# Kernel optimization log

Hardware: AMD Instinct MI355X
Metric: run time of the kernel (lower is better)

Reference implementation:

```python
import jax, jax.numpy as jnp
import numpy as np

B, S, HID = 2, 2048, 3584
H, KV, D = 16, 8, 256
RQ, RK, RV = 6, 2, 2
GRP = H // KV
EPS = 1e-6
SOFTCAP = 50.0
SCALE = 256.0 ** -0.5  # query_pre_attn_scalar ** -0.5
NEG = -2.3819763e38


def _rmsnorm(x, w):
    # Gemma RMSNorm: fp32 normalize, scale by (1 + weight)
    xf = x.astype(jnp.float32)
    n = xf * jax.lax.rsqrt(jnp.mean(xf * xf, axis=-1, keepdims=True) + EPS)
    return (n * (1.0 + w)).astype(x.dtype)


def _rope_factor(x, freqs_cis):
    # x: [B,S,R,D]; freqs_cis: [S, D/2, 2] = (cos, sin)
    h = D // 2
    cos = freqs_cis[None, :, None, :, 0]  # [1,S,1,D/2]
    sin = freqs_cis[None, :, None, :, 1]
    x1, x2 = x[..., :h], x[..., h:]
    return jnp.concatenate([x1 * cos - x2 * sin, x2 * cos + x1 * sin], axis=-1)


def setup_inputs() -> dict:
    key = jax.random.key(0)
    ks = jax.random.split(key, 10)
    hidden_states = jax.random.normal(ks[0], (B, S, HID), dtype=jnp.float32)
    # rotary tables
    pos = jnp.arange(S, dtype=jnp.float32)
    inv = 1.0 / (10000.0 ** (jnp.arange(0, D, 2, dtype=jnp.float32) / D))
    ang = pos[:, None] * inv[None, :]                     # [S, D/2]
    freqs_cis = jnp.stack([jnp.cos(ang), jnp.sin(ang)], axis=-1)  # [S,D/2,2]
    kv_write_indices = jnp.arange(S, dtype=jnp.int32)
    k_cache_A = jnp.zeros((B, S, KV, RK), jnp.float32)
    k_cache_B = jnp.zeros((B, S, RK, D), jnp.float32)
    v_cache_A = jnp.zeros((B, S, KV, RV), jnp.float32)
    v_cache_B = jnp.zeros((B, S, RV, D), jnp.float32)
    causal = jnp.tril(jnp.ones((S, S), bool))
    mask = jnp.where(causal, 0.0, NEG)[None, None].astype(jnp.float32)
    sd = 1.0 / np.sqrt(HID)
    W_A_q = jax.random.normal(ks[1], (HID, H * RQ), jnp.float32) * sd
    W_A_k = jax.random.normal(ks[2], (HID, KV * RK), jnp.float32) * sd
    W_A_v = jax.random.normal(ks[3], (HID, KV * RV), jnp.float32) * sd
    W_B_q = jax.random.normal(ks[4], (HID, RQ * D), jnp.float32) * sd
    W_B_k = jax.random.normal(ks[5], (HID, RK * D), jnp.float32) * sd
    W_B_v = jax.random.normal(ks[6], (HID, RV * D), jnp.float32) * sd
    o_proj_w = jax.random.normal(ks[7], (H * D, HID), jnp.float32) * (1.0 / np.sqrt(H * D))
    q_norm_w = jnp.zeros((D,), jnp.float32)
    k_norm_w = jnp.zeros((D,), jnp.float32)
    return dict(hidden_states=hidden_states, freqs_cis=freqs_cis,
                kv_write_indices=kv_write_indices,
                k_cache_A=k_cache_A, k_cache_B=k_cache_B,
                v_cache_A=v_cache_A, v_cache_B=v_cache_B, mask=mask,
                W_A_q=W_A_q, W_A_k=W_A_k, W_A_v=W_A_v,
                W_B_q=W_B_q, W_B_k=W_B_k, W_B_v=W_B_v,
                o_proj_w=o_proj_w, q_norm_w=q_norm_w, k_norm_w=k_norm_w)


def reference(hidden_states, freqs_cis, kv_write_indices,
              k_cache_A, k_cache_B, v_cache_A, v_cache_B, mask,
              W_A_q, W_A_k, W_A_v, W_B_q, W_B_k, W_B_v,
              o_proj_w, q_norm_w, k_norm_w):
    hs = hidden_states
    # rank-factor projections (many small GEMMs)
    A_q = (hs @ W_A_q).reshape(B, S, H, RQ)
    A_k = (hs @ W_A_k).reshape(B, S, KV, RK)
    A_v = (hs @ W_A_v).reshape(B, S, KV, RV)
    B_q = (hs @ W_B_q).reshape(B, S, RQ, D)
    B_k = (hs @ W_B_k).reshape(B, S, RK, D)
    B_v = (hs @ W_B_v).reshape(B, S, RV, D)
    # qk-norm on low-rank B factors
    B_q = _rmsnorm(B_q, q_norm_w)
    B_k = _rmsnorm(B_k, k_norm_w)
    # RoPE on factors
    B_q = _rope_factor(B_q, freqs_cis)
    B_k = _rope_factor(B_k, freqs_cis)
    # factored KV cache write (prefill: indices = arange(S))
    kA = k_cache_A.at[:, kv_write_indices].set(A_k)
    kB = k_cache_B.at[:, kv_write_indices].set(B_k)
    vA = v_cache_A.at[:, kv_write_indices].set(A_v)
    vB = v_cache_B.at[:, kv_write_indices].set(B_v)
    # reconstruct Q/K/V from rank-R tensor products, divided by rank
    Q = jnp.einsum('bshr,bsrd->bshd', A_q.astype(jnp.float32),
                   B_q.astype(jnp.float32)) / RQ          # [B,S,H,D]
    K = jnp.einsum('bskr,bsrd->bskd', kA, kB) / RK        # [B,S,KV,D]
    V = jnp.einsum('bskr,bsrd->bskd', vA, vB) / RV
    Q = Q.astype(hs.dtype)
    # GQA expand
    K = jnp.repeat(K, GRP, axis=2)
    V = jnp.repeat(V, GRP, axis=2)
    q = jnp.transpose(Q, (0, 2, 1, 3)) * SCALE            # [B,H,S,D]
    k = jnp.transpose(K, (0, 2, 1, 3))
    v = jnp.transpose(V, (0, 2, 1, 3))
    scores = jnp.einsum('bhqd,bhkd->bhqk', q, k).astype(jnp.float32)
    scores = SOFTCAP * jnp.tanh(scores / SOFTCAP)
    scores = scores + mask
    probs = jax.nn.softmax(scores, axis=-1).astype(q.dtype)
    out = jnp.einsum('bhqk,bhkd->bhqd', probs, v)         # [B,H,S,D]
    out = jnp.transpose(out, (0, 2, 1, 3)).reshape(B, S, H * D)
    return out @ o_proj_w
```

## Files before the change

kernel.cpp:

```cpp
#include <hip/hip_runtime.h>

#define B_    2
#define S_    2048
#define HID_  3584
#define H_    16
#define KV_   8
#define D_    256
#define RQ_   6
#define NPROJ 2688
#define HD_   4096
#define MTOK  4096
#define EPS_  1e-6f
#define NEG_  -2.3819763e38f
#define SCALE_ 0.0625f

typedef unsigned short u16;
typedef __attribute__((ext_vector_type(8))) short short8;
typedef __attribute__((ext_vector_type(4))) float f32x4;

__device__ __forceinline__ u16 f2bf(float f) {
  unsigned u = __float_as_uint(f);
  u += 0x7fffu + ((u >> 16) & 1u);
  return (u16)(u >> 16);
}

__device__ __forceinline__ float b2f(u16 b) {
  return __uint_as_float(((unsigned)b) << 16);
}

__device__ __forceinline__ void gl_lds16(const void* g, void* l) {
  __builtin_amdgcn_global_load_lds((__attribute__((address_space(1))) void*)g,
                                   (__attribute__((address_space(3))) void*)l, 16, 0, 0);
}

__global__ __launch_bounds__(256) void cvt_f32_bf16(const float* __restrict__ src,
                                                    u16* __restrict__ dst, int n) {
  int i = blockIdx.x * 256 + threadIdx.x;
  const int stride = gridDim.x * 256;
  const int n4 = n >> 2;
  for (; i < n4; i += stride) {
    float4 v = ((const float4*)src)[i];
    ushort4 o;
    o.x = f2bf(v.x); o.y = f2bf(v.y); o.z = f2bf(v.z); o.w = f2bf(v.w);
    ((ushort4*)dst)[i] = o;
  }
}

__global__ __launch_bounds__(256) void transpose_f32_bf16(const float* __restrict__ src,
                                                          u16* __restrict__ dst, int R, int C) {
  __shared__ float tile[32][33];
  const int tx = threadIdx.x & 31, ty = threadIdx.x >> 5;
  const int r0 = blockIdx.x << 5, c0 = blockIdx.y << 5;
#pragma unroll
  for (int j = 0; j < 4; ++j) {
    int r = r0 + ty + j * 8, c = c0 + tx;
    tile[ty + j * 8][tx] = (r < R && c < C) ? src[(size_t)r * C + c] : 0.f;
  }
  __syncthreads();
#pragma unroll
  for (int j = 0; j < 4; ++j) {
    int cc = c0 + ty + j * 8, rr = r0 + tx;
    if (cc < C && rr < R) dst[(size_t)cc * R + rr] = f2bf(tile[tx][ty + j * 8]);
  }
}

__global__ __launch_bounds__(256) void transpose_multi(
    const float* __restrict__ s0, const float* __restrict__ s1,
    const float* __restrict__ s2, const float* __restrict__ s3,
    const float* __restrict__ s4, const float* __restrict__ s5,
    u16* __restrict__ WT) {
  const int y = blockIdx.y;
  const float* src; int cofs, C, c0;
  if      (y < 3)  { src = s0; cofs = 0;    C = 96;   c0 = y << 5; }
  else if (y < 4)  { src = s1; cofs = 96;   C = 16;   c0 = 0; }
  else if (y < 5)  { src = s2; cofs = 112;  C = 16;   c0 = 0; }
  else if (y < 53) { src = s3; cofs = 128;  C = 1536; c0 = (y - 5) << 5; }
  else if (y < 69) { src = s4; cofs = 1664; C = 512;  c0 = (y - 53) << 5; }
  else             { src = s5; cofs = 2176; C = 512;  c0 = (y - 69) << 5; }
  u16* dst = WT + (size_t)cofs * HID_;
  __shared__ float tile[32][33];
  const int tx = threadIdx.x & 31, ty = threadIdx.x >> 5;
  const int r0 = blockIdx.x << 5;
#pragma unroll
  for (int j = 0; j < 4; ++j) {
    int r = r0 + ty + j * 8, c = c0 + tx;
    tile[ty + j * 8][tx] = (c < C) ? src[(size_t)r * C + c] : 0.f;
  }
  __syncthreads();
#pragma unroll
  for (int j = 0; j < 4; ++j) {
    int cc = c0 + ty + j * 8, rr = r0 + tx;
    if (cc < C) dst[(size_t)cc * HID_ + rr] = f2bf(tile[tx][ty + j * 8]);
  }
}

__global__ __launch_bounds__(256) void transpose_bf16_b(const u16* __restrict__ src,
                                                        u16* __restrict__ dst, int R, int C) {
  __shared__ u16 tile[32][34];
  const size_t plane = (size_t)R * C;
  const u16* s = src + (size_t)blockIdx.z * plane;
  u16* d = dst + (size_t)blockIdx.z * plane;
  const int tx = threadIdx.x & 31, ty = threadIdx.x >> 5;
  const int r0 = blockIdx.x << 5, c0 = blockIdx.y << 5;
#pragma unroll
  for (int j = 0; j < 4; ++j) {
    int r = r0 + ty + j * 8, c = c0 + tx;
    tile[ty + j * 8][tx] = (r < R && c < C) ? s[(size_t)r * C + c] : (u16)0;
  }
  __syncthreads();
#pragma unroll
  for (int j = 0; j < 4; ++j) {
    int cc = c0 + ty + j * 8, rr = r0 + tx;
    if (cc < C && rr < R) d[(size_t)cc * R + rr] = tile[tx][ty + j * 8];
  }
}

__global__ __launch_bounds__(512, 1)
void gemm256(const u16* __restrict__ A, const u16* __restrict__ Bm, void* __restrict__ Cv,
             int N, int lda, int ldb, int ldc, int NT, int GY, int obf) {
  __shared__ __align__(16) u16 ring[4][2][8192];
  const int t = threadIdx.x;
  const int lane = t & 63;
  const int lq = lane & 15, lg = lane >> 4;
  const int w = t >> 6;
  const int wm = w >> 2, wn = w & 3;

  const int wg = blockIdx.x;
  const int chunk = gridDim.x >> 3;
  const int gid = (wg & 7) * chunk + (wg >> 3);
  const int bm0 = (gid / GY) * 256, bn0 = (gid % GY) * 256;

  const int rsub = lane >> 2;
  const int ksub = (((lane & 3) ^ ((lane >> 3) & 3)) << 3);
  const u16* paw = A + (size_t)(bm0 + w * 32 + rsub) * lda + ksub;
  const u16* pbw = Bm + (size_t)(bn0 + w * 32 + rsub) * ldb + ksub;

  const int rdo = lq * 32 + ((lg ^ ((lq >> 1) & 3)) << 3);

  f32x4 zero = {0.f, 0.f, 0.f, 0.f};
  f32x4 acc[8][4];
#pragma unroll
  for (int m = 0; m < 8; ++m)
#pragma unroll
    for (int n = 0; n < 4; ++n) acc[m][n] = zero;

#define STAGE_(T)                                                              \
  {                                                                            \
    const int slot_ = (T) & 3;                                                 \
    const size_t ko_ = (size_t)(T) * 32;                                       \
    gl_lds16(paw + ko_,            &ring[slot_][0][(2 * w + 0) * 512]);        \
    gl_lds16(paw + 16 * lda + ko_, &ring[slot_][0][(2 * w + 1) * 512]);        \
    gl_lds16(pbw + ko_,            &ring[slot_][1][(2 * w + 0) * 512]);        \
    gl_lds16(pbw + 16 * ldb + ko_, &ring[slot_][1][(2 * w + 1) * 512]);        \
  }

  STAGE_(0);
  STAGE_(1);
  STAGE_(2);
  asm volatile("s_waitcnt vmcnt(8)" ::: "memory");
  __builtin_amdgcn_s_barrier();

  for (int T = 0; T < NT; ++T) {
    __builtin_amdgcn_sched_barrier(0);
    const int s = T & 3;
    const u16* as = &ring[s][0][wm * 4096];
    const u16* bs = &ring[s][1][wn * 2048];
    short8 af[8], bf[4];
#pragma unroll
    for (int m = 0; m < 8; ++m) af[m] = *(const short8*)(as + m * 512 + rdo);
#pragma unroll
    for (int n = 0; n < 4; ++n) bf[n] = *(const short8*)(bs + n * 512 + rdo);
    if (T + 3 < NT) STAGE_(T + 3);
    __builtin_amdgcn_s_setprio(1);
#pragma unroll
    for (int m = 0; m < 8; ++m)
#pragma unroll
      for (int n = 0; n < 4; ++n)
        acc[m][n] = __builtin_amdgcn_mfma_f32_16x16x32_bf16(af[m], bf[n], acc[m][n], 0, 0, 0);
    __builtin_amdgcn_s_setprio(0);
    if (T + 3 < NT)      { asm volatile("s_waitcnt vmcnt(8) lgkmcnt(0)" ::: "memory"); }
    else if (T + 2 < NT) { asm volatile("s_waitcnt vmcnt(4) lgkmcnt(0)" ::: "memory"); }
    else if (T + 1 < NT) { asm volatile("s_waitcnt vmcnt(0) lgkmcnt(0)" ::: "memory"); }
    else                 { asm volatile("s_waitcnt lgkmcnt(0)" ::: "memory"); }
    __builtin_amdgcn_s_barrier();
  }
#undef STAGE_

#pragma unroll
  for (int m = 0; m < 8; ++m) {
    const int row = bm0 + wm * 128 + m * 16 + lg * 4;
#pragma unroll
    for (int n = 0; n < 4; ++n) {
      const int col = bn0 + wn * 64 + n * 16 + lq;
      if (col < N) {
        if (obf) {
          u16* cp = (u16*)Cv + (size_t)row * ldc + col;
          cp[0] = f2bf(acc[m][n][0]);
          cp[(size_t)ldc] = f2bf(acc[m][n][1]);
          cp[(size_t)2 * ldc] = f2bf(acc[m][n][2]);
          cp[(size_t)3 * ldc] = f2bf(acc[m][n][3]);
        } else {
          float* cp = (float*)Cv + (size_t)row * ldc + col;
          cp[0] = acc[m][n][0];
          cp[(size_t)ldc] = acc[m][n][1];
          cp[(size_t)2 * ldc] = acc[m][n][2];
          cp[(size_t)3 * ldc] = acc[m][n][3];
        }
      }
    }
  }
}

__global__ __launch_bounds__(256)
void build_qkv(const u16* __restrict__ P, const float* __restrict__ freqs,
               const float* __restrict__ qw, const float* __restrict__ kw,
               u16* __restrict__ Qg, u16* __restrict__ Kg, u16* __restrict__ Vg) {
  const int token = blockIdx.x;
  const int b = token >> 11, s = token & 2047;
  const int d = threadIdx.x;
  const u16* row = P + (size_t)token * NPROJ;
  __shared__ float aL[128];
  __shared__ float rQ[6][256];
  __shared__ float rK[2][256];
  __shared__ float red[4][8];

  if (d < 128) aL[d] = b2f(row[d]);
  float bq[6], bk[2], bv[2];
#pragma unroll
  for (int r = 0; r < 6; ++r) bq[r] = b2f(row[128 + r * 256 + d]);
#pragma unroll
  for (int r = 0; r < 2; ++r) bk[r] = b2f(row[1664 + r * 256 + d]);
#pragma unroll
  for (int r = 0; r < 2; ++r) bv[r] = b2f(row[2176 + r * 256 + d]);

  float sq[8];
#pragma unroll
  for (int r = 0; r < 6; ++r) sq[r] = bq[r] * bq[r];
  sq[6] = bk[0] * bk[0];
  sq[7] = bk[1] * bk[1];
#pragma unroll
  for (int j = 0; j < 8; ++j) {
    sq[j] += __shfl_xor(sq[j], 32, 64);
    sq[j] += __shfl_xor(sq[j], 16, 64);
    sq[j] += __shfl_xor(sq[j], 8, 64);
    sq[j] += __shfl_xor(sq[j], 4, 64);
    sq[j] += __shfl_xor(sq[j], 2, 64);
    sq[j] += __shfl_xor(sq[j], 1, 64);
  }
  const int lane = d & 63, wv = d >> 6;
  if (lane == 0) {
#pragma unroll
    for (int j = 0; j < 8; ++j) red[wv][j] = sq[j];
  }
  __syncthreads();
  float inv[8];
#pragma unroll
  for (int j = 0; j < 8; ++j) {
    float ss = red[0][j] + red[1][j] + red[2][j] + red[3][j];
    inv[j] = rsqrtf(ss * (1.0f / 256.0f) + EPS_);
  }
  const float gq = 1.f + qw[d], gk = 1.f + kw[d];
#pragma unroll
  for (int r = 0; r < 6; ++r) rQ[r][d] = bq[r] * inv[r] * gq;
#pragma unroll
  for (int r = 0; r < 2; ++r) rK[r][d] = bk[r] * inv[6 + r] * gk;
  __syncthreads();

  const int dh = d & 127;
  const float co = freqs[(s * 128 + dh) * 2 + 0];
  const float sn = freqs[(s * 128 + dh) * 2 + 1];
  float q_ro[6], k_ro[2];
  if (d < 128) {
#pragma unroll
    for (int r = 0; r < 6; ++r) q_ro[r] = rQ[r][d] * co - rQ[r][d + 128] * sn;
#pragma unroll
    for (int r = 0; r < 2; ++r) k_ro[r] = rK[r][d] * co - rK[r][d + 128] * sn;
  } else {
#pragma unroll
    for (int r = 0; r < 6; ++r) q_ro[r] = rQ[r][d] * co + rQ[r][d - 128] * sn;
#pragma unroll
    for (int r = 0; r < 2; ++r) k_ro[r] = rK[r][d] * co + rK[r][d - 128] * sn;
  }
  const float qs = SCALE_ * (1.0f / 6.0f);
#pragma unroll
  for (int h = 0; h < 16; ++h) {
    float a = 0.f;
#pragma unroll
    for (int r = 0; r < 6; ++r) a += aL[h * 6 + r] * q_ro[r];
    Qg[((size_t)(b * H_ + h) * S_ + s) * D_ + d] = f2bf(a * qs);
  }
#pragma unroll
  for (int kv = 0; kv < 8; ++kv) {
    float ak = aL[96 + kv * 2] * k_ro[0] + aL[96 + kv * 2 + 1] * k_ro[1];
    Kg[((size_t)(b * KV_ + kv) * S_ + s) * D_ + d] = f2bf(ak * 0.5f);
    float av = aL[112 + kv * 2] * bv[0] + aL[112 + kv * 2 + 1] * bv[1];
    Vg[((size_t)(b * KV_ + kv) * S_ + s) * D_ + d] = f2bf(av * 0.5f);
  }
}

__global__ __launch_bounds__(256, 2)
void attn_kernel(const u16* __restrict__ Qg, const u16* __restrict__ Kg,
                 const u16* __restrict__ VTg, u16* __restrict__ Og) {
  __shared__ __align__(16) u16 Kbuf[2][8192];
  __shared__ __align__(16) u16 Vbuf[2][8192];
  __shared__ __align__(16) u16 Pbuf[4][512];

  const int t = threadIdx.x;
  const int lane = t & 63;
  const int lq = lane & 15, lg = lane >> 4;
  const int qw = t >> 6;
  const int h = blockIdx.x, b = blockIdx.y;
  const int qt = 31 - blockIdx.z;
  const int q0 = qt * 64;
  const int kvh = h >> 1;

  const u16* Kplane = Kg + (size_t)(b * KV_ + kvh) * S_ * D_;
  const u16* VTplane = VTg + (size_t)(b * KV_ + kvh) * D_ * S_;

  const int qg = q0 + qw * 16 + lq;
  const u16* Qrow = Qg + ((size_t)(b * H_ + h) * S_ + qg) * D_;
  short8 qf[8];
#pragma unroll
  for (int ks = 0; ks < 8; ++ks) qf[ks] = *(const short8*)(Qrow + ks * 32 + lg * 8);

  int ksrc[4], vsrc[4];
#pragma unroll
  for (int i = 0; i < 4; ++i) {
    const int kr = i * 8 + (t >> 5);
    ksrc[i] = kr * D_ + (((t & 31) ^ (kr & 7)) << 3);
    const int vr = i * 64 + (t >> 2);
    vsrc[i] = vr * S_ + (((t & 3) ^ ((vr >> 1) & 3)) << 3);
  }

  f32x4 zero = {0.f, 0.f, 0.f, 0.f};
  f32x4 oacc[16];
#pragma unroll
  for (int db = 0; db < 16; ++db) oacc[db] = zero;
  float m_s = NEG_, l_s = 0.f;

  const int qro = q0 + qw * 16 + lg * 4;
  const int nt = 2 * (qt + 1);

#pragma unroll
  for (int i = 0; i < 4; ++i) {
    gl_lds16(Kplane + ksrc[i], &Kbuf[0][0] + (i * 256 + t) * 8);
    gl_lds16(VTplane + vsrc[i], &Vbuf[0][0] + (i * 256 + t) * 8);
  }
  __syncthreads();
  int cur = 0;
  for (int it = 0; it < nt; ++it) {
    const int kv0 = it * 32;
    if (it + 1 < nt) {
      const u16* kp = Kplane + (size_t)(it + 1) * 32 * D_;
      const u16* vp = VTplane + (it + 1) * 32;
      u16* kd = &Kbuf[cur ^ 1][0];
      u16* vd = &Vbuf[cur ^ 1][0];
#pragma unroll
      for (int i = 0; i < 4; ++i) {
        gl_lds16(kp + ksrc[i], kd + (i * 256 + t) * 8);
        gl_lds16(vp + vsrc[i], vd + (i * 256 + t) * 8);
      }
    }
    const u16* Kb = &Kbuf[cur][0];
    f32x4 sacc[2];
    sacc[0] = zero; sacc[1] = zero;
    __builtin_amdgcn_s_setprio(1);
#pragma unroll
    for (int kb = 0; kb < 2; ++kb) {
      const int rbase = (kb * 16 + lq) * 256;
      const int sw = lq & 7;
#pragma unroll
      for (int ks = 0; ks < 8; ++ks) {
        short8 kf = *(const short8*)(Kb + rbase + (((ks * 4 + lg) ^ sw) << 3));
        sacc[kb] = __builtin_amdgcn_mfma_f32_16x16x32_bf16(kf, qf[ks], sacc[kb], 0, 0, 0);
      }
    }
    __builtin_amdgcn_s_setprio(0);
    const bool tail = (it >= 2 * qt);
#pragma unroll
    for (int kb = 0; kb < 2; ++kb)
#pragma unroll
      for (int r = 0; r < 4; ++r) {
        float x = sacc[kb][r];
        const float e = __expf(-fabsf(x) * 0.04f);
        const float th = (1.f - e) * __builtin_amdgcn_rcpf(1.f + e);
        x = copysignf(50.0f * th, x);
        if (tail && (kv0 + kb * 16 + lg * 4 + r > qg)) x = NEG_;
        sacc[kb][r] = x;
      }
    float vmax = fmaxf(fmaxf(fmaxf(sacc[0][0], sacc[0][1]), fmaxf(sacc[0][2], sacc[0][3])),
                       fmaxf(fmaxf(sacc[1][0], sacc[1][1]), fmaxf(sacc[1][2], sacc[1][3])));
    vmax = fmaxf(vmax, __shfl_xor(vmax, 16, 64));
    vmax = fmaxf(vmax, __shfl_xor(vmax, 32, 64));
    if (__any(vmax > m_s + 8.f)) {
      const float mn = fmaxf(m_s, vmax);
      const float c = __expf(m_s - mn);
      m_s = mn;
      l_s *= c;
      float c4[4];
#pragma unroll
      for (int r = 0; r < 4; ++r) c4[r] = __shfl(c, lg * 4 + r, 16);
#pragma unroll
      for (int db = 0; db < 16; ++db) {
        oacc[db][0] *= c4[0]; oacc[db][1] *= c4[1];
        oacc[db][2] *= c4[2]; oacc[db][3] *= c4[3];
      }
    }
    float ps = 0.f;
#pragma unroll
    for (int kb = 0; kb < 2; ++kb)
#pragma unroll
      for (int r = 0; r < 4; ++r) {
        const float p = __expf(sacc[kb][r] - m_s);
        sacc[kb][r] = p;
        ps += p;
      }
    ps += __shfl_xor(ps, 16, 64);
    ps += __shfl_xor(ps, 32, 64);
    l_s += ps;
    u16* Pw = &Pbuf[qw][0];
#pragma unroll
    for (int kb = 0; kb < 2; ++kb) {
      ushort4 pk;
      pk.x = f2bf(sacc[kb][0]); pk.y = f2bf(sacc[kb][1]);
      pk.z = f2bf(sacc[kb][2]); pk.w = f2bf(sacc[kb][3]);
      *(ushort4*)(Pw + 8 * lq + 128 * (2 * kb + (lg >> 1)) + 4 * (lg & 1)) = pk;
    }
    short8 pf = *(const short8*)(Pw + lane * 8);
    const u16* Vb = &Vbuf[cur][0];
    __builtin_amdgcn_s_setprio(1);
#pragma unroll
    for (int db = 0; db < 16; ++db) {
      const int d = db * 16 + lq;
      short8 vf = *(const short8*)(Vb + d * 32 + ((lg ^ ((lq >> 1) & 3)) << 3));
      oacc[db] = __builtin_amdgcn_mfma_f32_16x16x32_bf16(pf, vf, oacc[db], 0, 0, 0);
    }
    __builtin_amdgcn_s_setprio(0);
    __syncthreads();
    cur ^= 1;
  }
  const float invl = __builtin_amdgcn_rcpf(l_s);
  float inv4[4];
#pragma unroll
  for (int r = 0; r < 4; ++r) inv4[r] = __shfl(invl, lg * 4 + r, 16);
#pragma unroll
  for (int r = 0; r < 4; ++r) {
    u16* orow = Og + (size_t)(b * S_ + qro + r) * HD_ + h * D_;
#pragma unroll
    for (int db = 0; db < 16; ++db) orow[db * 16 + lq] = f2bf(oacc[db][r] * inv4[r]);
  }
}

extern "C" void kernel_launch(void* const* d_in, const int* in_sizes, int n_in,
                              void* d_out, int out_size, void* d_ws, size_t ws_size,
                              hipStream_t stream) {
  const float* hs    = (const float*)d_in[0];
  const float* freqs = (const float*)d_in[1];
  const float* W_A_q = (const float*)d_in[8];
  const float* W_A_k = (const float*)d_in[9];
  const float* W_A_v = (const float*)d_in[10];
  const float* W_B_q = (const float*)d_in[11];
  const float* W_B_k = (const float*)d_in[12];
  const float* W_B_v = (const float*)d_in[13];
  const float* Wo    = (const float*)d_in[14];
  const float* qw    = (const float*)d_in[15];
  const float* kw    = (const float*)d_in[16];
  float* out = (float*)d_out;

  char* ws = (char*)d_ws;
  u16* hsb = (u16*)(ws);
  u16* WT  = (u16*)(ws + 29360128);
  u16* WoT = (u16*)(ws + 48627712);
  u16* Qg  = (u16*)(ws + 77987840);
  u16* Kg  = (u16*)(ws + 111542272);
  u16* Vg  = (u16*)(ws + 128319488);
  u16* VTg = (u16*)(ws + 145096704);
  u16* AOg = (u16*)(ws + 161873920);
  u16* Pb  = (u16*)d_out;

  cvt_f32_bf16<<<1024, 256, 0, stream>>>(hs, hsb, MTOK * HID_);
  transpose_multi<<<dim3(112, 85), 256, 0, stream>>>(W_A_q, W_A_k, W_A_v, W_B_q, W_B_k, W_B_v, WT);
  transpose_f32_bf16<<<dim3(128, 112), 256, 0, stream>>>(Wo, WoT, HD_, HID_);

  gemm256<<<176, 512, 0, stream>>>(hsb, WT, Pb, NPROJ, HID_, HID_, NPROJ, 112, 11, 1);
  build_qkv<<<4096, 256, 0, stream>>>(Pb, freqs, qw, kw, Qg, Kg, Vg);
  transpose_bf16_b<<<dim3(64, 8, 16), 256, 0, stream>>>(Vg, VTg, S_, D_);
  attn_kernel<<<dim3(16, 2, 32), 256, 0, stream>>>(Qg, Kg, VTg, AOg);
  gemm256<<<224, 512, 0, stream>>>(AOg, WoT, out, HID_, HD_, HD_, HID_, 128, 14, 0);
}
```

Baseline: 418.9 us.

## Pass P fragments via cross-lane shuffles and split attention launch in halves

The softmax probabilities are now converted to bf16 with packed hardware conversion and rearranged into the MFMA A-operand layout with lane shuffles, instead of a round trip through a per-wave LDS buffer. This removes an LDS write/read and the shared Pbuf allocation on every KV tile. The attention launch is also split into two launches over head halves using a head offset argument, which changes scheduling and adds a second launch overhead.

After: 515.5 us. 23.1% more time.

```diff
diff --git a/kernel.cpp b/kernel.cpp
--- a/kernel.cpp
+++ b/kernel.cpp
@@ -300,16 +300,15 @@
 
 __global__ __launch_bounds__(256, 2)
 void attn_kernel(const u16* __restrict__ Qg, const u16* __restrict__ Kg,
-                 const u16* __restrict__ VTg, u16* __restrict__ Og) {
+                 const u16* __restrict__ VTg, u16* __restrict__ Og, int h0) {
   __shared__ __align__(16) u16 Kbuf[2][8192];
   __shared__ __align__(16) u16 Vbuf[2][8192];
-  __shared__ __align__(16) u16 Pbuf[4][512];
 
   const int t = threadIdx.x;
   const int lane = t & 63;
   const int lq = lane & 15, lg = lane >> 4;
   const int qw = t >> 6;
-  const int h = blockIdx.x, b = blockIdx.y;
+  const int h = blockIdx.x + h0, b = blockIdx.y;
   const int qt = 31 - blockIdx.z;
   const int q0 = qt * 64;
   const int kvh = h >> 1;
@@ -340,6 +339,10 @@
 
   const int qro = q0 + qw * 16 + lg * 4;
   const int nt = 2 * (qt + 1);
+
+  const int s0l = ((lg & 1) << 5) + lq;
+  const int s1l = s0l + 16;
+  const bool hi = ((lg >> 1) & 1) != 0;
 
 #pragma unroll
   for (int i = 0; i < 4; ++i) {
@@ -418,15 +421,21 @@
     ps += __shfl_xor(ps, 16, 64);
     ps += __shfl_xor(ps, 32, 64);
     l_s += ps;
-    u16* Pw = &Pbuf[qw][0];
-#pragma unroll
-    for (int kb = 0; kb < 2; ++kb) {
-      ushort4 pk;
-      pk.x = f2bf(sacc[kb][0]); pk.y = f2bf(sacc[kb][1]);
-      pk.z = f2bf(sacc[kb][2]); pk.w = f2bf(sacc[kb][3]);
-      *(ushort4*)(Pw + 8 * lq + 128 * (2 * kb + (lg >> 1)) + 4 * (lg & 1)) = pk;
-    }
-    short8 pf = *(const short8*)(Pw + lane * 8);
+    unsigned A0, A1, B0, B1;
+    asm("v_cvt_pk_bf16_f32 %0, %1, %2" : "=v"(A0) : "v"(sacc[0][0]), "v"(sacc[0][1]));
+    asm("v_cvt_pk_bf16_f32 %0, %1, %2" : "=v"(A1) : "v"(sacc[0][2]), "v"(sacc[0][3]));
+    asm("v_cvt_pk_bf16_f32 %0, %1, %2" : "=v"(B0) : "v"(sacc[1][0]), "v"(sacc[1][1]));
+    asm("v_cvt_pk_bf16_f32 %0, %1, %2" : "=v"(B1) : "v"(sacc[1][2]), "v"(sacc[1][3]));
+    const unsigned xa0 = __shfl((int)A0, s0l, 64), xb0 = __shfl((int)B0, s0l, 64);
+    const unsigned xa1 = __shfl((int)A1, s0l, 64), xb1 = __shfl((int)B1, s0l, 64);
+    const unsigned ya0 = __shfl((int)A0, s1l, 64), yb0 = __shfl((int)B0, s1l, 64);
+    const unsigned ya1 = __shfl((int)A1, s1l, 64), yb1 = __shfl((int)B1, s1l, 64);
+    union { unsigned u[4]; short8 v; } pu;
+    pu.u[0] = hi ? xb0 : xa0;
+    pu.u[1] = hi ? xb1 : xa1;
+    pu.u[2] = hi ? yb0 : ya0;
+    pu.u[3] = hi ? yb1 : ya1;
+    const short8 pf = pu.v;
     const u16* Vb = &Vbuf[cur][0];
     __builtin_amdgcn_s_setprio(1);
 #pragma unroll
@@ -485,6 +494,7 @@
   gemm256<<<176, 512, 0, stream>>>(hsb, WT, Pb, NPROJ, HID_, HID_, NPROJ, 112, 11, 1);
   build_qkv<<<4096, 256, 0, stream>>>(Pb, freqs, qw, kw, Qg, Kg, Vg);
   transpose_bf16_b<<<dim3(64, 8, 16), 256, 0, stream>>>(Vg, VTg, S_, D_);
-  attn_kernel<<<dim3(16, 2, 32), 256, 0, stream>>>(Qg, Kg, VTg, AOg);
+  attn_kernel<<<dim3(8, 2, 32), 256, 0, stream>>>(Qg, Kg, VTg, AOg, 0);
+  attn_kernel<<<dim3(8, 2, 32), 256, 0, stream>>>(Qg, Kg, VTg, AOg, 8);
   gemm256<<<224, 512, 0, stream>>>(AOg, WoT, out, HID_, HD_, HD_, HID_, 128, 14, 0);
 }
```
